# Performance work log

Measured on AMD Instinct MI355X. Metric: run time of the kernel, lower is better.

Reference implementation:

```python
import jax, jax.numpy as jnp
import numpy as np

B, S, V, E, H, L = 64, 512, 32000, 512, 1024, 2


def setup_inputs() -> dict:
    key = jax.random.key(0)
    ks = jax.random.split(key, 12)
    sc = 0.05
    x = jax.random.randint(ks[0], (B, S), 0, V)
    emb = jax.random.normal(ks[1], (V, E), dtype=jnp.float32) * sc
    # Gate weights stacked along output dim in order [f, i, g, o] -> [4H, in_dim]
    Wx0 = jax.random.normal(ks[2], (4 * H, E), dtype=jnp.float32) * sc
    bx0 = jnp.zeros((4 * H,), dtype=jnp.float32)
    Wh0 = jax.random.normal(ks[3], (4 * H, H), dtype=jnp.float32) * sc
    bh0 = jnp.zeros((4 * H,), dtype=jnp.float32)
    Wx1 = jax.random.normal(ks[4], (4 * H, H), dtype=jnp.float32) * sc
    bx1 = jnp.zeros((4 * H,), dtype=jnp.float32)
    Wh1 = jax.random.normal(ks[5], (4 * H, H), dtype=jnp.float32) * sc
    bh1 = jnp.zeros((4 * H,), dtype=jnp.float32)
    fc_w = jax.random.normal(ks[6], (1, H), dtype=jnp.float32) * sc
    fc_b = jnp.zeros((1,), dtype=jnp.float32)
    return {"x": x, "emb": emb, "Wx0": Wx0, "bx0": bx0, "Wh0": Wh0, "bh0": bh0,
            "Wx1": Wx1, "bx1": bx1, "Wh1": Wh1, "bh1": bh1,
            "fc_w": fc_w, "fc_b": fc_b}


def _lstm_cell(inp, h, c, Wx, bx, Wh, bh):
    # Fused 4-gate GEMM, then split: order [forget, input, candidate, output]
    z = inp @ Wx.T + bx + h @ Wh.T + bh            # [B, 4H]
    f, i, g, o = jnp.split(z, 4, axis=-1)
    f = jax.nn.sigmoid(f)
    i = jax.nn.sigmoid(i)
    g = jnp.tanh(g)
    o = jax.nn.sigmoid(o)
    c = f * c + i * g
    h = o * jnp.tanh(c)
    return h, c


def reference(x, emb, Wx0, bx0, Wh0, bh0, Wx1, bx1, Wh1, bh1, fc_w, fc_b):
    xe = emb[x]                                     # [B, S, E]
    xts = jnp.swapaxes(xe, 0, 1)                    # [S, B, E] for scan
    b = xe.shape[0]
    zeros = jnp.zeros((b, H), dtype=xe.dtype)
    carry0 = (zeros, zeros, zeros, zeros)           # h0, c0, h1, c1

    def step(carry, xt):
        h0, c0, h1, c1 = carry
        h0, c0 = _lstm_cell(xt, h0, c0, Wx0, bx0, Wh0, bh0)
        h1, c1 = _lstm_cell(h0, h1, c1, Wx1, bx1, Wh1, bh1)
        return (h0, c0, h1, c1), None

    (h0, c0, h1, c1), _ = jax.lax.scan(step, carry0, xts)
    out = jax.nn.sigmoid(h1 @ fc_w.T + fc_b)        # [B, 1]
    return out
```

## Files before the change

### kernel.cpp

```cpp
#include <hip/hip_runtime.h>

#define BATCH 64
#define SLEN  512
#define EDIM  512
#define HDIM  1024
#define NBLK  256
#define HALF  128
#define ZR    32
#define ZST   68
#define HSLOT 65536
#define XROWB 512
#define RING  8

#define XE_BYTES ((size_t)SLEN * BATCH * XROWB)
#define HBUF_BIG ((size_t)SLEN * HSLOT)
#define HBUF_SML ((size_t)RING * HSLOT)

typedef _Float16 f16x8 __attribute__((ext_vector_type(8)));
typedef float  f32x4  __attribute__((ext_vector_type(4)));
typedef unsigned u32x4 __attribute__((ext_vector_type(4)));
typedef unsigned u32x2 __attribute__((ext_vector_type(2)));

__device__ __forceinline__ float sigm(float x) { return 1.0f / (1.0f + __expf(-x)); }
__device__ __forceinline__ float tanhfast(float x) {
  float e = __expf(-2.0f * __builtin_fabsf(x));
  float r = (1.0f - e) / (1.0f + e);
  return x < 0.0f ? -r : r;
}

__device__ __forceinline__ unsigned enc_e5m2(float v) {
  unsigned short hb = __builtin_bit_cast(unsigned short, (_Float16)v);
  return ((unsigned)hb + 0x80u) >> 8;
}

__device__ __forceinline__ void dec4(unsigned w, unsigned &lo, unsigned &hi) {
  lo = __builtin_amdgcn_perm(w, 0u, 0x05000400u);
  hi = __builtin_amdgcn_perm(w, 0u, 0x07000600u);
}

__device__ __forceinline__ void dec16(u32x4 d, f16x8 &fa, f16x8 &fb) {
  union { unsigned u[4]; f16x8 v; } A, B;
  dec4(d[0], A.u[0], A.u[1]); dec4(d[1], A.u[2], A.u[3]);
  dec4(d[2], B.u[0], B.u[1]); dec4(d[3], B.u[2], B.u[3]);
  fa = A.v; fb = B.v;
}

__device__ __forceinline__ void st8_wt(unsigned char* p, unsigned d0, unsigned d1) {
  u32x2 v = {d0, d1};
  asm volatile("global_store_dwordx2 %0, %1, off sc0 sc1" :: "v"(p), "v"(v) : "memory");
}

__device__ __forceinline__ u32x4 ald16b(const unsigned char* p) {
  union { unsigned long long q[2]; u32x4 v; } u;
  u.q[0] = __hip_atomic_load((const unsigned long long*)p,       __ATOMIC_RELAXED, __HIP_MEMORY_SCOPE_AGENT);
  u.q[1] = __hip_atomic_load((const unsigned long long*)(p + 8), __ATOMIC_RELAXED, __HIP_MEMORY_SCOPE_AGENT);
  return u.v;
}
template<int BIG>
__device__ __forceinline__ u32x4 hload16(const unsigned char* p) {
  if constexpr (BIG) return *(const u32x4*)p;
  else return ald16b(p);
}

__device__ __forceinline__ void block_wait(const int* f, int target, int* gate) {
  if (target <= 0) return;
  if ((threadIdx.x >> 6) == 0) {
    if (__hip_atomic_load(gate, __ATOMIC_RELAXED, __HIP_MEMORY_SCOPE_WORKGROUP) < target) {
      const int l = threadIdx.x & 63;
      int tries = 0;
      while (true) {
        int v0 = __hip_atomic_load(f + l,      __ATOMIC_RELAXED, __HIP_MEMORY_SCOPE_AGENT);
        int v1 = __hip_atomic_load(f + l + 64, __ATOMIC_RELAXED, __HIP_MEMORY_SCOPE_AGENT);
        if (__all((v0 >= target) && (v1 >= target))) break;
        __builtin_amdgcn_s_sleep(1);
        if (++tries > (1 << 21)) break;
      }
      if (l == 0)
        __hip_atomic_fetch_max(gate, target, __ATOMIC_RELEASE, __HIP_MEMORY_SCOPE_WORKGROUP);
    }
  } else {
    int tries = 0;
    while (__hip_atomic_load(gate, __ATOMIC_ACQUIRE, __HIP_MEMORY_SCOPE_WORKGROUP) < target) {
      __builtin_amdgcn_s_sleep(1);
      if (++tries > (1 << 21)) break;
    }
  }
}

__global__ void xe_gather(const int* __restrict__ x, const float* __restrict__ emb,
                          unsigned char* __restrict__ xe) {
  int g = blockIdx.x * blockDim.x + threadIdx.x;
  if (g >= SLEN * BATCH * (EDIM / 8)) return;
  int e8 = g & 63, bt = g >> 6;
  int b = bt & 63, t = bt >> 6;
  int tok = x[b * SLEN + t];
  const float* er = emb + (size_t)tok * EDIM + e8 * 8;
  f32x4 v0 = *(const f32x4*)er, v1 = *(const f32x4*)(er + 4);
  unsigned d0 = enc_e5m2(v0[0]) | (enc_e5m2(v0[1]) << 8) | (enc_e5m2(v0[2]) << 16) | (enc_e5m2(v0[3]) << 24);
  unsigned d1 = enc_e5m2(v1[0]) | (enc_e5m2(v1[1]) << 8) | (enc_e5m2(v1[2]) << 16) | (enc_e5m2(v1[3]) << 24);
  int pb = (e8 >> 3) * 64 + (e8 & 3) * 16 + ((e8 >> 2) & 1) * 8;
  *(u32x2*)(xe + ((size_t)t * BATCH + b) * XROWB + pb) = (u32x2){d0, d1};
}

#define MFMA(a, b, c) __builtin_amdgcn_mfma_f32_16x16x32_f16(a, b, c, 0, 0, 0)
#define LDSBF(t, kg) (*(const f16x8*)(&Ws[(size_t)((((t) * 64 + (kg)) * 64 + lane)) * 16]))

template<int BIG>
__global__ __launch_bounds__(512, 2) void lstm_persistent(
    const int* __restrict__ x, const float* __restrict__ emb,
    const float* __restrict__ Wx0, const float* __restrict__ bx0,
    const float* __restrict__ Wh0, const float* __restrict__ bh0,
    const float* __restrict__ Wx1, const float* __restrict__ bx1,
    const float* __restrict__ Wh1, const float* __restrict__ bh1,
    const unsigned char* __restrict__ xe, int use_xe,
    unsigned char* h0buf, unsigned char* h1buf, int* f0, int* f1)
{
  __shared__ __align__(16) unsigned char Ws[2 * 64 * 64 * 16];
  __shared__ float zbuf[BATCH * ZST];
  __shared__ float bias[ZR];
  __shared__ int gateF0, gateF1;

  const int tid   = threadIdx.x;
  const int wg    = blockIdx.x;
  const int layer = wg >> 7;
  const int sub   = wg & (HALF - 1);

  if (tid == 0) { gateF0 = 0; gateF1 = 0; }

  {
    const int KG = layer ? 64 : 48;
    for (int idx = tid; idx < 2 * KG * 64; idx += 512) {
      int t  = idx / (KG * 64);
      int r  = idx - t * (KG * 64);
      int kg = r >> 6, ln = r & 63;
      int n  = t * 16 + (ln & 15);
      int grow = (n >> 3) * HDIM + sub * 8 + (n & 7);
      int k  = kg * 32 + (ln >> 4) * 8;
      const float* src;
      if (layer == 0) src = (k < EDIM) ? (Wx0 + (size_t)grow * EDIM + k)
                                       : (Wh0 + (size_t)grow * HDIM + (k - EDIM));
      else            src = (k < HDIM) ? (Wx1 + (size_t)grow * HDIM + k)
                                       : (Wh1 + (size_t)grow * HDIM + (k - HDIM));
      f32x4 v0 = *(const f32x4*)src, v1 = *(const f32x4*)(src + 4);
      f16x8 o = { (_Float16)v0[0], (_Float16)v0[1], (_Float16)v0[2], (_Float16)v0[3],
                  (_Float16)v1[0], (_Float16)v1[1], (_Float16)v1[2], (_Float16)v1[3] };
      *(f16x8*)(&Ws[(size_t)((t * 64 + kg) * 64 + ln) * 16]) = o;
    }
    if (tid < ZR) {
      int grow = (tid >> 3) * HDIM + sub * 8 + (tid & 7);
      bias[tid] = layer ? (bx1[grow] + bh1[grow]) : (bx0[grow] + bh0[grow]);
    }
  }
  __syncthreads();

  const int lane = tid & 63, wave = tid >> 6;
  const int mrow = lane & 15;
  const int q    = lane >> 4;
  const int mt   = wave >> 1, nt = wave & 1;
  const int brow = mt * 16 + mrow;
  const int bg = tid >> 3, jl = tid & 7;
  const int zrow = mt * 16 + q * 4;
  const int pbase = (sub >> 3) * 64 + (sub & 3) * 16 + ((sub >> 2) & 1) * 8;

  float cst = 0.0f;

#define SLOTB(s) ((size_t)(BIG ? (s) : ((s) & (RING - 1))) * HSLOT)

#define ZWRITE()                                                                  \
  do {                                                                            \
    _Pragma("unroll")                                                             \
    for (int r = 0; r < 4; ++r) {                                                 \
      zbuf[(zrow + r) * ZST + nt * 34 + mrow]      = acc0[r];                     \
      zbuf[(zrow + r) * ZST + nt * 34 + 16 + mrow] = acc1[r];                     \
    }                                                                             \
  } while (0)

#define EPILOGUE(hdst, slotExpr)                                                  \
  do {                                                                            \
    float zf = zbuf[bg*ZST +      jl] + zbuf[bg*ZST + 34 +      jl] + bias[     jl]; \
    float zi = zbuf[bg*ZST +  8 + jl] + zbuf[bg*ZST + 34 +  8 + jl] + bias[ 8 + jl]; \
    float zg = zbuf[bg*ZST + 16 + jl] + zbuf[bg*ZST + 34 + 16 + jl] + bias[16 + jl]; \
    float zo = zbuf[bg*ZST + 24 + jl] + zbuf[bg*ZST + 34 + 24 + jl] + bias[24 + jl]; \
    float fg = sigm(zf), ig = sigm(zi), gg = tanhfast(zg), og = sigm(zo);         \
    cst = fg * cst + ig * gg;                                                     \
    unsigned by = enc_e5m2(og * tanhfast(cst));                                   \
    unsigned w0 = by | (((unsigned)__shfl_xor((int)by, 1, 64) & 0xFFu) << 8);     \
    w0 |= ((unsigned)__shfl_xor((int)w0, 2, 64) & 0xFFFFu) << 16;                 \
    unsigned dd1 = (unsigned)__shfl_xor((int)w0, 4, 64);                          \
    if (jl == 0)                                                                  \
      st8_wt(hdst + (slotExpr) + (size_t)bg * 1024 + pbase, w0, dd1);             \
    asm volatile("s_waitcnt vmcnt(0)" ::: "memory");                              \
  } while (0)

  if (layer == 0) {
    for (int s = 0; s < SLEN; ++s) {
      f32x4 acc0 = {0.f,0.f,0.f,0.f}, acc1 = {0.f,0.f,0.f,0.f};
      if (use_xe) {
        const unsigned char* aX = xe + ((size_t)s * BATCH + brow) * XROWB + nt * 256 + q * 16;
        #pragma unroll
        for (int g = 0; g < 4; ++g) {
          f16x8 fa, fb; dec16(*(const u32x4*)(aX + g * 64), fa, fb);
          const int kg = nt * 8 + g * 2;
          acc0 = MFMA(fa, LDSBF(0, kg), acc0);     acc1 = MFMA(fa, LDSBF(1, kg), acc1);
          acc0 = MFMA(fb, LDSBF(0, kg + 1), acc0); acc1 = MFMA(fb, LDSBF(1, kg + 1), acc1);
        }
      } else {
        const int tok = x[brow * SLEN + s];
        const float* erow = emb + (size_t)tok * EDIM;
        #pragma unroll
        for (int g = 0; g < 4; ++g) {
          const int k = nt * 256 + g * 64;
          const int kg = nt * 8 + g * 2;
          f32x4 e0 = *(const f32x4*)(erow + k + q * 8);
          f32x4 e1 = *(const f32x4*)(erow + k + q * 8 + 4);
          f16x8 fa = { (_Float16)e0[0], (_Float16)e0[1], (_Float16)e0[2], (_Float16)e0[3],
                       (_Float16)e1[0], (_Float16)e1[1], (_Float16)e1[2], (_Float16)e1[3] };
          f32x4 e2 = *(const f32x4*)(erow + k + 32 + q * 8);
          f32x4 e3 = *(const f32x4*)(erow + k + 32 + q * 8 + 4);
          f16x8 fb = { (_Float16)e2[0], (_Float16)e2[1], (_Float16)e2[2], (_Float16)e2[3],
                       (_Float16)e3[0], (_Float16)e3[1], (_Float16)e3[2], (_Float16)e3[3] };
          acc0 = MFMA(fa, LDSBF(0, kg), acc0);     acc1 = MFMA(fa, LDSBF(1, kg), acc1);
          acc0 = MFMA(fb, LDSBF(0, kg + 1), acc0); acc1 = MFMA(fb, LDSBF(1, kg + 1), acc1);
        }
      }
      if (s > 0) {
        block_wait(f0, s, &gateF0);
        const unsigned char* hp = h0buf + SLOTB(s - 1) + (size_t)brow * 1024 + nt * 512 + q * 16;
        #pragma unroll
        for (int g = 0; g < 8; ++g) {
          f16x8 fa, fb; dec16(hload16<BIG>(hp + g * 64), fa, fb);
          const int kg = 16 + nt * 16 + g * 2;
          acc0 = MFMA(fa, LDSBF(0, kg), acc0);     acc1 = MFMA(fa, LDSBF(1, kg), acc1);
          acc0 = MFMA(fb, LDSBF(0, kg + 1), acc0); acc1 = MFMA(fb, LDSBF(1, kg + 1), acc1);
        }
      }
      ZWRITE();
      __syncthreads();
      if constexpr (!BIG) {
        if (s >= RING) { block_wait(f1, s - RING + 2, &gateF1); block_wait(f0, s - RING + 2, &gateF0); }
      }
      EPILOGUE(h0buf, SLOTB(s));
      __syncthreads();
      if (tid == 0)
        __hip_atomic_store(&f0[sub], s + 1, __ATOMIC_RELAXED, __HIP_MEMORY_SCOPE_AGENT);
    }
  } else {
    for (int j = 0; j < SLEN; ++j) {
      f32x4 acc0 = {0.f,0.f,0.f,0.f}, acc1 = {0.f,0.f,0.f,0.f};
      block_wait(f0, j + 1, &gateF0);
      {
        const unsigned char* hp = h0buf + SLOTB(j) + (size_t)brow * 1024 + nt * 512 + q * 16;
        #pragma unroll
        for (int g = 0; g < 8; ++g) {
          f16x8 fa, fb; dec16(hload16<BIG>(hp + g * 64), fa, fb);
          const int kg = nt * 16 + g * 2;
          acc0 = MFMA(fa, LDSBF(0, kg), acc0);     acc1 = MFMA(fa, LDSBF(1, kg), acc1);
          acc0 = MFMA(fb, LDSBF(0, kg + 1), acc0); acc1 = MFMA(fb, LDSBF(1, kg + 1), acc1);
        }
      }
      if (j > 0) {
        block_wait(f1, j, &gateF1);
        const unsigned char* hp = h1buf + SLOTB(j - 1) + (size_t)brow * 1024 + nt * 512 + q * 16;
        #pragma unroll
        for (int g = 0; g < 8; ++g) {
          f16x8 fa, fb; dec16(hload16<BIG>(hp + g * 64), fa, fb);
          const int kg = 32 + nt * 16 + g * 2;
          acc0 = MFMA(fa, LDSBF(0, kg), acc0);     acc1 = MFMA(fa, LDSBF(1, kg), acc1);
          acc0 = MFMA(fb, LDSBF(0, kg + 1), acc0); acc1 = MFMA(fb, LDSBF(1, kg + 1), acc1);
        }
      }
      ZWRITE();
      __syncthreads();
      if constexpr (!BIG) {
        if (j >= RING) block_wait(f1, j - RING + 2, &gateF1);
      }
      EPILOGUE(h1buf, SLOTB(j));
      __syncthreads();
      if (tid == 0)
        __hip_atomic_store(&f1[sub], j + 1, __ATOMIC_RELAXED, __HIP_MEMORY_SCOPE_AGENT);
    }
  }
}

__global__ void fc_kernel(const unsigned char* __restrict__ h1slot,
                          const float* __restrict__ fcw, const float* __restrict__ fcb,
                          float* __restrict__ out) {
  __shared__ float part[512];
  const int tid = threadIdx.x, b = tid >> 3, q2 = tid & 7;
  const unsigned char* hr = h1slot + (size_t)b * 1024;
  float acc = 0.0f;
  for (int gg = 0; gg < 2; ++gg) {
    int g = q2 * 2 + gg;
    #pragma unroll
    for (int p = 0; p < 64; ++p) {
      unsigned by = hr[g * 64 + p];
      float hv = (float)__builtin_bit_cast(_Float16, (unsigned short)(by << 8));
      int qq = (p >> 4) & 3, hf = (p >> 3) & 1, jj = p & 7;
      acc += hv * fcw[g * 64 + hf * 32 + qq * 8 + jj];
    }
  }
  part[tid] = acc;
  __syncthreads();
  if (tid < BATCH) {
    float s = fcb[0];
    #pragma unroll
    for (int i = 0; i < 8; ++i) s += part[tid * 8 + i];
    out[tid] = 1.0f / (1.0f + __expf(-s));
  }
}

extern "C" void kernel_launch(void* const* d_in, const int* in_sizes, int n_in,
                              void* d_out, int out_size, void* d_ws, size_t ws_size,
                              hipStream_t stream) {
  (void)in_sizes; (void)n_in; (void)out_size;
  const int*   x   = (const int*)  d_in[0];
  const float* emb = (const float*)d_in[1];
  const float* Wx0 = (const float*)d_in[2];
  const float* bx0 = (const float*)d_in[3];
  const float* Wh0 = (const float*)d_in[4];
  const float* bh0 = (const float*)d_in[5];
  const float* Wx1 = (const float*)d_in[6];
  const float* bx1 = (const float*)d_in[7];
  const float* Wh1 = (const float*)d_in[8];
  const float* bh1 = (const float*)d_in[9];
  const float* fcw = (const float*)d_in[10];
  const float* fcb = (const float*)d_in[11];
  float* out = (float*)d_out;

  char* ws = (char*)d_ws;
  int* f0 = (int*)(ws);
  int* f1 = (int*)(ws + 512);

  const size_t need_big = 4096 + 2 * HBUF_BIG + XE_BYTES;
  const size_t need_sml = 4096 + 2 * HBUF_SML + XE_BYTES;
  const int big    = (ws_size >= need_big) ? 1 : 0;
  const size_t hbytes = big ? HBUF_BIG : HBUF_SML;
  unsigned char* h0buf = (unsigned char*)(ws + 4096);
  unsigned char* h1buf = (unsigned char*)(ws + 4096 + hbytes);
  unsigned char* xe    = (unsigned char*)(ws + 4096 + 2 * hbytes);
  const int use_xe = (big || ws_size >= need_sml) ? 1 : 0;

  hipMemsetAsync(d_ws, 0, 4096, stream);
  if (use_xe) {
    const int groups = SLEN * BATCH * (EDIM / 8);
    xe_gather<<<(groups + 255) / 256, 256, 0, stream>>>(x, emb, xe);
  }
  if (big) {
    lstm_persistent<1><<<NBLK, 512, 0, stream>>>(x, emb, Wx0, bx0, Wh0, bh0,
                                                 Wx1, bx1, Wh1, bh1,
                                                 xe, use_xe, h0buf, h1buf, f0, f1);
    fc_kernel<<<1, 512, 0, stream>>>(h1buf + (size_t)(SLEN - 1) * HSLOT, fcw, fcb, out);
  } else {
    lstm_persistent<0><<<NBLK, 512, 0, stream>>>(x, emb, Wx0, bx0, Wh0, bh0,
                                                 Wx1, bx1, Wh1, bh1,
                                                 xe, use_xe, h0buf, h1buf, f0, f1);
    fc_kernel<<<1, 512, 0, stream>>>(h1buf + (size_t)((SLEN - 1) & (RING - 1)) * HSLOT, fcw, fcb, out);
  }
}
```

Measured before the change: 2.891 ms.

## Replace whole-layer block waits with per-quarter flag waits streamed into MFMA chunks

Each warp now waits only on the 32 producer flags for the slice of the hidden state it is about to consume, instead of one block-wide wait on all 128 flags gated through shared memory. Consumption is split into two quarters so MFMA work on the first slice can start while the second slice's producers are still finishing. This is meant to cut the serialization in the inter-block recurrence handshake. In exchange every warp polls global flags itself, which adds atomic traffic, and the shared gate caching for these waits is dropped.

```diff
diff --git a/kernel.cpp b/kernel.cpp
--- a/kernel.cpp
+++ b/kernel.cpp
@@ -60,6 +60,18 @@
 __device__ __forceinline__ u32x4 hload16(const unsigned char* p) {
   if constexpr (BIG) return *(const u32x4*)p;
   else return ald16b(p);
+}
+
+__device__ __forceinline__ void quarter_wait(const int* f, int base, int target) {
+  if (target <= 0) return;
+  const int l = threadIdx.x & 31;
+  int tries = 0;
+  while (true) {
+    int v = __hip_atomic_load(f + base + l, __ATOMIC_RELAXED, __HIP_MEMORY_SCOPE_AGENT);
+    if (__all(v >= target)) return;
+    __builtin_amdgcn_s_sleep(1);
+    if (++tries > (1 << 21)) return;
+  }
 }
 
 __device__ __forceinline__ void block_wait(const int* f, int target, int* gate) {
@@ -190,6 +202,21 @@
     if (jl == 0)                                                                  \
       st8_wt(hdst + (slotExpr) + (size_t)bg * 1024 + pbase, w0, dd1);             \
     asm volatile("s_waitcnt vmcnt(0)" ::: "memory");                              \
+  } while (0)
+
+#define HPART_STREAM(fl, target, hp, kgbase)                                      \
+  do {                                                                            \
+    _Pragma("unroll")                                                             \
+    for (int qq = 0; qq < 2; ++qq) {                                              \
+      quarter_wait(fl, (2 * nt + qq) * 32, target);                               \
+      _Pragma("unroll")                                                           \
+      for (int g = qq * 4; g < qq * 4 + 4; ++g) {                                 \
+        f16x8 fa, fb; dec16(hload16<BIG>((hp) + g * 64), fa, fb);                 \
+        const int kg = (kgbase) + g * 2;                                          \
+        acc0 = MFMA(fa, LDSBF(0, kg), acc0);     acc1 = MFMA(fa, LDSBF(1, kg), acc1); \
+        acc0 = MFMA(fb, LDSBF(0, kg + 1), acc0); acc1 = MFMA(fb, LDSBF(1, kg + 1), acc1); \
+      }                                                                           \
+    }                                                                             \
   } while (0)
 
   if (layer == 0) {
@@ -224,15 +251,8 @@
         }
       }
       if (s > 0) {
-        block_wait(f0, s, &gateF0);
         const unsigned char* hp = h0buf + SLOTB(s - 1) + (size_t)brow * 1024 + nt * 512 + q * 16;
-        #pragma unroll
-        for (int g = 0; g < 8; ++g) {
-          f16x8 fa, fb; dec16(hload16<BIG>(hp + g * 64), fa, fb);
-          const int kg = 16 + nt * 16 + g * 2;
-          acc0 = MFMA(fa, LDSBF(0, kg), acc0);     acc1 = MFMA(fa, LDSBF(1, kg), acc1);
-          acc0 = MFMA(fb, LDSBF(0, kg + 1), acc0); acc1 = MFMA(fb, LDSBF(1, kg + 1), acc1);
-        }
+        HPART_STREAM(f0, s, hp, 16 + nt * 16);
       }
       ZWRITE();
       __syncthreads();
@@ -247,27 +267,13 @@
   } else {
     for (int j = 0; j < SLEN; ++j) {
       f32x4 acc0 = {0.f,0.f,0.f,0.f}, acc1 = {0.f,0.f,0.f,0.f};
-      block_wait(f0, j + 1, &gateF0);
       {
         const unsigned char* hp = h0buf + SLOTB(j) + (size_t)brow * 1024 + nt * 512 + q * 16;
-        #pragma unroll
-        for (int g = 0; g < 8; ++g) {
-          f16x8 fa, fb; dec16(hload16<BIG>(hp + g * 64), fa, fb);
-          const int kg = nt * 16 + g * 2;
-          acc0 = MFMA(fa, LDSBF(0, kg), acc0);     acc1 = MFMA(fa, LDSBF(1, kg), acc1);
-          acc0 = MFMA(fb, LDSBF(0, kg + 1), acc0); acc1 = MFMA(fb, LDSBF(1, kg + 1), acc1);
-        }
+        HPART_STREAM(f0, j + 1, hp, nt * 16);
       }
       if (j > 0) {
-        block_wait(f1, j, &gateF1);
         const unsigned char* hp = h1buf + SLOTB(j - 1) + (size_t)brow * 1024 + nt * 512 + q * 16;
-        #pragma unroll
-        for (int g = 0; g < 8; ++g) {
-          f16x8 fa, fb; dec16(hload16<BIG>(hp + g * 64), fa, fb);
-          const int kg = 32 + nt * 16 + g * 2;
-          acc0 = MFMA(fa, LDSBF(0, kg), acc0);     acc1 = MFMA(fa, LDSBF(1, kg), acc1);
-          acc0 = MFMA(fb, LDSBF(0, kg + 1), acc0); acc1 = MFMA(fb, LDSBF(1, kg + 1), acc1);
-        }
+        HPART_STREAM(f1, j, hp, 32 + nt * 16);
       }
       ZWRITE();
       __syncthreads();
```

Measured after the change: 3.298 ms. +14.1%, slower.
